# Performance work log

Hardware: AMD Instinct MI355X
Metric: run time of the kernel (lower is better)

The kernel has to match this reference:

```python
import jax, jax.numpy as jnp
import numpy as np

B, L, H, W, C = 2, 32, 16, 16, 32  # L must equal channels for the view() to be consistent
CH = L  # conv channel count


def setup_inputs() -> dict:
    key = jax.random.key(0)
    k1, k2, k3, k4, k5 = jax.random.split(key, 5)
    return {
        "inputs": jax.random.normal(k1, (B, L, H, W, C), dtype=jnp.float32),
        "W1": jax.random.normal(k2, (CH // 2, CH), dtype=jnp.float32) * 0.1,
        "b1": jax.random.normal(k3, (CH // 2,), dtype=jnp.float32) * 0.1,
        "W2": jax.random.normal(k4, (CH, CH), dtype=jnp.float32) * 0.1,
        "b2": jax.random.normal(k5, (CH,), dtype=jnp.float32) * 0.1,
        "gamma": jnp.ones((1,), dtype=jnp.float32),
    }


def reference(inputs, W1, b1, W2, b2, gamma):
    b, l, h, w, c = inputs.shape
    n = l * h * w  # flattened 'spatial' positions after the (buggy-but-faithful) reshape
    # conv1x1 over dim-1 (torch Conv3d treats dim-1 as channels)
    x1 = jnp.einsum('ol,blhwc->bohwc', W1, inputs) + b1[None, :, None, None, None]
    # permute (0,4,1,2,3) then view(b, c//2, l*h*w)
    x1 = jnp.transpose(x1, (0, 4, 1, 2, 3)).reshape(b, c // 2, n)
    # attn[b, i, j] = sum_k x1[b, k, i] * x1[b, k, j]; softmax over last dim
    attn = jax.nn.softmax(jnp.einsum('bki,bkj->bij', x1, x1), axis=-1)  # [b, n, n]
    x2 = jnp.einsum('ol,blhwc->bohwc', W2, inputs) + b2[None, :, None, None, None]
    x2 = jnp.transpose(x2, (0, 4, 1, 2, 3)).reshape(b, c, n)
    # x2 @ attn^T : out[b, c, i] = sum_j x2[b, c, j] * attn[b, i, j]
    out = jnp.einsum('bcj,bij->bci', x2, attn)
    out = jnp.transpose(out.reshape(b, c, l, h, w), (0, 2, 3, 4, 1))
    return out * gamma + inputs
```

## Files before the change

kernel.cpp:

```cpp
#include <hip/hip_runtime.h>
#include <hip/hip_bf16.h>
#include <math.h>

typedef __bf16 bf16x8 __attribute__((ext_vector_type(8)));
typedef __bf16 bf16x4v __attribute__((ext_vector_type(4)));
typedef short  s16x4  __attribute__((ext_vector_type(4)));
typedef float  floatx16 __attribute__((ext_vector_type(16)));

#define KQ_ELEMS (2 * 8192 * 16)
#define PART_OFF 1572864
#define SQRT_LOG2E 1.2011224087864498f

__global__ __launch_bounds__(256) void proj_kernel(
    const float* __restrict__ in, const float* __restrict__ W1,
    const float* __restrict__ b1, const float* __restrict__ W2,
    const float* __restrict__ b2,
    __hip_bfloat16* __restrict__ Kq, __hip_bfloat16* __restrict__ Vswz)
{
    __shared__ float Xs[32][32];
    __shared__ float W1s[16 * 32];
    __shared__ float W2s[32 * 32];
    const int t = threadIdx.x;
    const int bid = blockIdx.x;
    const int b = bid >> 8;
    const int hw = bid & 255;

    {
        int l = t >> 3, cs = (t & 7) * 4;
        float4 v = *(const float4*)(in + (((size_t)b * 32 + l) * 256 + hw) * 32 + cs);
        *(float4*)&Xs[l][cs] = v;
    }
    if (t < 128) *(float4*)&W1s[t * 4] = *(const float4*)(W1 + t * 4);
    *(float4*)&W2s[t * 4] = *(const float4*)(W2 + t * 4);
    __syncthreads();

    const int c = t & 31;
    const int g = t >> 5;

#pragma unroll
    for (int oo = 0; oo < 2; ++oo) {
        int o = g * 2 + oo;
        float acc = b1[o];
#pragma unroll
        for (int l = 0; l < 32; ++l) acc += W1s[o * 32 + l] * Xs[l][c];
        int k = c >> 1;
        int i = (c & 1) * 4096 + o * 256 + hw;
        Kq[((size_t)b * 8192 + i) * 16 + k] = __float2bfloat16(acc * SQRT_LOG2E);
    }
#pragma unroll
    for (int oo = 0; oo < 4; ++oo) {
        int o = g * 4 + oo;
        float acc = b2[o];
#pragma unroll
        for (int l = 0; l < 32; ++l) acc += W2s[o * 32 + l] * Xs[l][c];
        int j = o * 256 + hw;
        int jt = j >> 5, rem = j & 31;
        int gg = rem >> 3, h = (rem >> 2) & 1, idx = rem & 3;
        Vswz[(size_t)b * 262144 + jt * 1024 + gg * 256 + h * 128 + c * 4 + idx] =
            __float2bfloat16(acc);
    }
}

__global__ __launch_bounds__(256) void flash_kernel(
    const __hip_bfloat16* __restrict__ Kq, const __hip_bfloat16* __restrict__ Vswz,
    float* __restrict__ Opart, float* __restrict__ Lpart, int lsplit)
{
    const int t = threadIdx.x;
    const int lane = t & 63;
    const int wv = t >> 6;
    const int m = lane & 31;
    const int h = lane >> 5;

    const int bid = blockIdx.x;
    const int split = 1 << lsplit;
    const int s = bid & (split - 1);
    const int itile = (bid >> lsplit) & 63;
    const int b = bid >> (lsplit + 6);
    const int i0 = itile * 128 + wv * 32;
    const int jcount = 8192 >> lsplit;
    const int niter = jcount >> 5;
    const int jt0 = (s * jcount) >> 5;

    const __hip_bfloat16* Kb = Kq + (size_t)b * 8192 * 16;
    const __hip_bfloat16* Vb = Vswz + (size_t)b * 262144 + h * 128 + m * 4;

    const bf16x8 bq = *(const bf16x8*)(Kb + (size_t)(i0 + m) * 16 + h * 8);

    floatx16 oa = {}, ob = {};
    float l0 = 0.f, l1 = 0.f, l2 = 0.f, l3 = 0.f;

    bf16x8 ak = *(const bf16x8*)(Kb + (size_t)(jt0 * 32 + m) * 16 + h * 8);
    s16x4 vf0 = *(const s16x4*)(Vb + (size_t)jt0 * 1024 + 0);
    s16x4 vf1 = *(const s16x4*)(Vb + (size_t)jt0 * 1024 + 256);
    s16x4 vf2 = *(const s16x4*)(Vb + (size_t)jt0 * 1024 + 512);
    s16x4 vf3 = *(const s16x4*)(Vb + (size_t)jt0 * 1024 + 768);

    for (int it = 0; it < niter; ++it) {
        const int jtn = jt0 + (it + 1 < niter ? it + 1 : it);
        bf16x8 ak_n = *(const bf16x8*)(Kb + (size_t)(jtn * 32 + m) * 16 + h * 8);
        s16x4 vn0 = *(const s16x4*)(Vb + (size_t)jtn * 1024 + 0);
        s16x4 vn1 = *(const s16x4*)(Vb + (size_t)jtn * 1024 + 256);
        s16x4 vn2 = *(const s16x4*)(Vb + (size_t)jtn * 1024 + 512);
        s16x4 vn3 = *(const s16x4*)(Vb + (size_t)jtn * 1024 + 768);

        floatx16 sc = __builtin_amdgcn_mfma_f32_32x32x16_bf16(ak, bq, (floatx16){}, 0, 0, 0);

#pragma unroll
        for (int g = 0; g < 4; ++g) {
            bf16x4v pb;
            float e0 = __builtin_amdgcn_exp2f(sc[4 * g + 0]);
            float e1 = __builtin_amdgcn_exp2f(sc[4 * g + 1]);
            float e2 = __builtin_amdgcn_exp2f(sc[4 * g + 2]);
            float e3 = __builtin_amdgcn_exp2f(sc[4 * g + 3]);
            l0 += e0; l1 += e1; l2 += e2; l3 += e3;
            pb[0] = (__bf16)e0; pb[1] = (__bf16)e1; pb[2] = (__bf16)e2; pb[3] = (__bf16)e3;
            s16x4 vf = (g == 0) ? vf0 : (g == 1) ? vf1 : (g == 2) ? vf2 : vf3;
            if (g < 2)
                oa = __builtin_amdgcn_mfma_f32_32x32x8bf16_1k(
                         __builtin_bit_cast(s16x4, pb), vf, oa, 0, 0, 0);
            else
                ob = __builtin_amdgcn_mfma_f32_32x32x8bf16_1k(
                         __builtin_bit_cast(s16x4, pb), vf, ob, 0, 0, 0);
        }
        ak = ak_n; vf0 = vn0; vf1 = vn1; vf2 = vn2; vf3 = vn3;
    }

    oa = oa + ob;
    float l = (l0 + l1) + (l2 + l3);
    l += __shfl_xor(l, 32);

#pragma unroll
    for (int r = 0; r < 16; ++r) {
        int iloc = (r & 3) + 8 * (r >> 2) + 4 * h;
        size_t row = (size_t)b * 8192 + i0 + iloc;
        Opart[((row << lsplit) | s) * 32 + m] = oa[r];
    }
    if (h == 0)
        Lpart[(((size_t)b * 8192 + i0 + m) << lsplit) | s] = l;
}

__global__ __launch_bounds__(256) void combine_kernel(
    const float* __restrict__ Opart, const float* __restrict__ Lpart,
    const float* __restrict__ in, const float* __restrict__ gamma,
    float* __restrict__ out, int lsplit)
{
    const int t = threadIdx.x;
    const int c = t & 31;
    const size_t row = (size_t)blockIdx.x * 8 + (t >> 5);
    const int split = 1 << lsplit;

    float acc = 0.f, l = 0.f;
    for (int s = 0; s < split; ++s) {
        acc += Opart[((row << lsplit) | s) * 32 + c];
        l += Lpart[(row << lsplit) | s];
    }
    size_t idx = row * 32 + c;
    out[idx] = (acc / l) * gamma[0] + in[idx];
}

extern "C" void kernel_launch(void* const* d_in, const int* in_sizes, int n_in,
                              void* d_out, int out_size, void* d_ws, size_t ws_size,
                              hipStream_t stream) {
    const float* in = (const float*)d_in[0];
    const float* W1 = (const float*)d_in[1];
    const float* b1 = (const float*)d_in[2];
    const float* W2 = (const float*)d_in[3];
    const float* b2 = (const float*)d_in[4];
    const float* gamma = (const float*)d_in[5];
    float* out = (float*)d_out;

    __hip_bfloat16* Kq = (__hip_bfloat16*)d_ws;
    __hip_bfloat16* Vswz = Kq + KQ_ELEMS;

    int lsplit = 3;
    while (lsplit > 1) {
        size_t need = (size_t)PART_OFF + ((size_t)16384 << lsplit) * 33 * 4;
        if (need <= ws_size) break;
        --lsplit;
    }
    float* Opart = (float*)((char*)d_ws + PART_OFF);
    float* Lpart = Opart + ((size_t)16384 << lsplit) * 32;

    proj_kernel<<<512, 256, 0, stream>>>(in, W1, b1, W2, b2, Kq, Vswz);
    flash_kernel<<<2 * 64 * (1 << lsplit), 256, 0, stream>>>(Kq, Vswz, Opart, Lpart, lsplit);
    combine_kernel<<<2048, 256, 0, stream>>>(Opart, Lpart, in, gamma, out, lsplit);
}
```

Measured before the change: 115.6 us.

## Accumulate split-K flash partials with atomics and raise split count

Replaces the per-split partial output buffers and the combine reduction with float atomic adds into a single accumulator. The proj kernel zeroes that accumulator. The split count is fixed at 16, doubling the flash grid to 2048 blocks. The intent is to remove the partial-buffer write/read traffic and expose more parallelism, at the cost of atomic contention (16 adders per element) and non-deterministic summation order.

```diff
diff --git a/kernel.cpp b/kernel.cpp
--- a/kernel.cpp
+++ b/kernel.cpp
@@ -8,14 +8,17 @@
 typedef float  floatx16 __attribute__((ext_vector_type(16)));
 
 #define KQ_ELEMS (2 * 8192 * 16)
-#define PART_OFF 1572864
+#define OACC_OFF 1572864
+#define ACC_FLOATS (16384 * 32 + 16384)
 #define SQRT_LOG2E 1.2011224087864498f
+#define LSPLIT 4
 
 __global__ __launch_bounds__(256) void proj_kernel(
     const float* __restrict__ in, const float* __restrict__ W1,
     const float* __restrict__ b1, const float* __restrict__ W2,
     const float* __restrict__ b2,
-    __hip_bfloat16* __restrict__ Kq, __hip_bfloat16* __restrict__ Vswz)
+    __hip_bfloat16* __restrict__ Kq, __hip_bfloat16* __restrict__ Vswz,
+    float* __restrict__ acc0)
 {
     __shared__ float Xs[32][32];
     __shared__ float W1s[16 * 32];
@@ -24,6 +27,13 @@
     const int bid = blockIdx.x;
     const int b = bid >> 8;
     const int hw = bid & 255;
+
+    {
+        int gid = bid * 256 + t;
+        *(float4*)(acc0 + (size_t)gid * 4) = make_float4(0.f, 0.f, 0.f, 0.f);
+        if (gid < 4096)
+            *(float4*)(acc0 + 524288 + (size_t)gid * 4) = make_float4(0.f, 0.f, 0.f, 0.f);
+    }
 
     {
         int l = t >> 3, cs = (t & 7) * 4;
@@ -63,7 +73,7 @@
 
 __global__ __launch_bounds__(256) void flash_kernel(
     const __hip_bfloat16* __restrict__ Kq, const __hip_bfloat16* __restrict__ Vswz,
-    float* __restrict__ Opart, float* __restrict__ Lpart, int lsplit)
+    float* __restrict__ Oacc, float* __restrict__ Lacc)
 {
     const int t = threadIdx.x;
     const int lane = t & 63;
@@ -72,14 +82,12 @@
     const int h = lane >> 5;
 
     const int bid = blockIdx.x;
-    const int split = 1 << lsplit;
-    const int s = bid & (split - 1);
-    const int itile = (bid >> lsplit) & 63;
-    const int b = bid >> (lsplit + 6);
+    const int s = bid & 15;
+    const int itile = (bid >> LSPLIT) & 63;
+    const int b = bid >> (LSPLIT + 6);
     const int i0 = itile * 128 + wv * 32;
-    const int jcount = 8192 >> lsplit;
-    const int niter = jcount >> 5;
-    const int jt0 = (s * jcount) >> 5;
+    const int niter = 512 >> 5;
+    const int jt0 = s * niter;
 
     const __hip_bfloat16* Kb = Kq + (size_t)b * 8192 * 16;
     const __hip_bfloat16* Vb = Vswz + (size_t)b * 262144 + h * 128 + m * 4;
@@ -87,7 +95,7 @@
     const bf16x8 bq = *(const bf16x8*)(Kb + (size_t)(i0 + m) * 16 + h * 8);
 
     floatx16 oa = {}, ob = {};
-    float l0 = 0.f, l1 = 0.f, l2 = 0.f, l3 = 0.f;
+    float2 l01 = {0.f, 0.f}, l23 = {0.f, 0.f};
 
     bf16x8 ak = *(const bf16x8*)(Kb + (size_t)(jt0 * 32 + m) * 16 + h * 8);
     s16x4 vf0 = *(const s16x4*)(Vb + (size_t)jt0 * 1024 + 0);
@@ -112,7 +120,7 @@
             float e1 = __builtin_amdgcn_exp2f(sc[4 * g + 1]);
             float e2 = __builtin_amdgcn_exp2f(sc[4 * g + 2]);
             float e3 = __builtin_amdgcn_exp2f(sc[4 * g + 3]);
-            l0 += e0; l1 += e1; l2 += e2; l3 += e3;
+            l01.x += e0; l01.y += e1; l23.x += e2; l23.y += e3;
             pb[0] = (__bf16)e0; pb[1] = (__bf16)e1; pb[2] = (__bf16)e2; pb[3] = (__bf16)e3;
             s16x4 vf = (g == 0) ? vf0 : (g == 1) ? vf1 : (g == 2) ? vf2 : vf3;
             if (g < 2)
@@ -126,36 +134,29 @@
     }
 
     oa = oa + ob;
-    float l = (l0 + l1) + (l2 + l3);
+    float l = (l01.x + l01.y) + (l23.x + l23.y);
     l += __shfl_xor(l, 32);
 
 #pragma unroll
     for (int r = 0; r < 16; ++r) {
         int iloc = (r & 3) + 8 * (r >> 2) + 4 * h;
         size_t row = (size_t)b * 8192 + i0 + iloc;
-        Opart[((row << lsplit) | s) * 32 + m] = oa[r];
+        unsafeAtomicAdd(&Oacc[row * 32 + m], oa[r]);
     }
     if (h == 0)
-        Lpart[(((size_t)b * 8192 + i0 + m) << lsplit) | s] = l;
+        unsafeAtomicAdd(&Lacc[(size_t)b * 8192 + i0 + m], l);
 }
 
-__global__ __launch_bounds__(256) void combine_kernel(
-    const float* __restrict__ Opart, const float* __restrict__ Lpart,
+__global__ __launch_bounds__(256) void finalize_kernel(
+    const float* __restrict__ Oacc, const float* __restrict__ Lacc,
     const float* __restrict__ in, const float* __restrict__ gamma,
-    float* __restrict__ out, int lsplit)
+    float* __restrict__ out)
 {
     const int t = threadIdx.x;
     const int c = t & 31;
     const size_t row = (size_t)blockIdx.x * 8 + (t >> 5);
-    const int split = 1 << lsplit;
-
-    float acc = 0.f, l = 0.f;
-    for (int s = 0; s < split; ++s) {
-        acc += Opart[((row << lsplit) | s) * 32 + c];
-        l += Lpart[(row << lsplit) | s];
-    }
     size_t idx = row * 32 + c;
-    out[idx] = (acc / l) * gamma[0] + in[idx];
+    out[idx] = (Oacc[idx] / Lacc[row]) * gamma[0] + in[idx];
 }
 
 extern "C" void kernel_launch(void* const* d_in, const int* in_sizes, int n_in,
@@ -171,17 +172,10 @@
 
     __hip_bfloat16* Kq = (__hip_bfloat16*)d_ws;
     __hip_bfloat16* Vswz = Kq + KQ_ELEMS;
+    float* Oacc = (float*)((char*)d_ws + OACC_OFF);
+    float* Lacc = Oacc + 16384 * 32;
 
-    int lsplit = 3;
-    while (lsplit > 1) {
-        size_t need = (size_t)PART_OFF + ((size_t)16384 << lsplit) * 33 * 4;
-        if (need <= ws_size) break;
-        --lsplit;
-    }
-    float* Opart = (float*)((char*)d_ws + PART_OFF);
-    float* Lpart = Opart + ((size_t)16384 << lsplit) * 32;
-
-    proj_kernel<<<512, 256, 0, stream>>>(in, W1, b1, W2, b2, Kq, Vswz);
-    flash_kernel<<<2 * 64 * (1 << lsplit), 256, 0, stream>>>(Kq, Vswz, Opart, Lpart, lsplit);
-    combine_kernel<<<2048, 256, 0, stream>>>(Opart, Lpart, in, gamma, out, lsplit);
+    proj_kernel<<<512, 256, 0, stream>>>(in, W1, b1, W2, b2, Kq, Vswz, Oacc);
+    flash_kernel<<<2 * 64 * (1 << LSPLIT), 256, 0, stream>>>(Kq, Vswz, Oacc, Lacc);
+    finalize_kernel<<<2048, 256, 0, stream>>>(Oacc, Lacc, in, gamma, out);
 }
```

After: 112.3 us. -2.8%, faster.
